# Kernel tuning notes

Measured on AMD Instinct MI355X. Metric: run time of the kernel, lower is better.

Reference implementation:

```python
import jax
jax.config.update("jax_enable_x64", True)  # hash math needs int64, as in the TF source
import jax.numpy as jnp
import numpy as np

NUM_LEVELS = 16
LEVEL_DIM = 2
BASE_RES = 16
HASHMAP_SIZE = 2 ** 19
N_POINTS = 1048576


def setup_inputs() -> dict:
    key = jax.random.key(0)
    k1, k2 = jax.random.split(key)
    # raw coords in [-size, size] with size=1.0 (forward normalizes to [0,1))
    x = jax.random.uniform(k1, (N_POINTS, 3), dtype=jnp.float32, minval=-1.0, maxval=1.0)
    # stacked per-level hash tables, init U(-1e-4, 1e-4) as in the keras layer
    tables = jax.random.uniform(
        k2, (NUM_LEVELS, HASHMAP_SIZE, LEVEL_DIM), dtype=jnp.float32,
        minval=-1e-4, maxval=1e-4)
    return {"x": x, "tables": tables}


def reference(x, tables):
    size = 1.0
    xn = jnp.clip((x + size) / (2.0 * size), 0.0, 1.0 - 1e-6)  # [N,3] in [0,1)
    primes = jnp.array([1546061, 1005013, 1673733], dtype=jnp.int64)  # per-axis hash primes
    offsets = jnp.array(
        [[0, 0, 0], [0, 0, 1], [0, 1, 0], [0, 1, 1],
         [1, 0, 0], [1, 0, 1], [1, 1, 0], [1, 1, 1]], dtype=jnp.int64)  # [8,3] cube corners
    is_one = offsets == 1  # [8,3]

    outs = []
    for lvl in range(NUM_LEVELS):  # fixed small unroll over resolution levels
        res = float(BASE_RES * (2 ** lvl))
        scaled = xn * res                      # [N,3]
        fl = jnp.floor(scaled)
        frac = scaled - fl                     # [N,3]
        corners = fl.astype(jnp.int64)[:, None, :] + offsets[None]      # [N,8,3]
        h = (jnp.sum(corners * primes, axis=-1) ^ lvl) % HASHMAP_SIZE   # [N,8]
        emb = tables[lvl][h]                   # gather -> [N,8,LEVEL_DIM]
        # trilinear weights: prod over axes of frac (if corner bit==1) else 1-frac
        w = jnp.prod(jnp.where(is_one[None], frac[:, None, :], 1.0 - frac[:, None, :]),
                     axis=-1)                  # [N,8]
        outs.append(jnp.sum(emb * w[..., None], axis=1))  # [N,LEVEL_DIM]
    return jnp.concatenate(outs, axis=-1)      # [N, NUM_LEVELS*LEVEL_DIM]
```

## Files before the change

### kernel.cpp

```cpp
#include <hip/hip_runtime.h>


#define NUM_LEVELS 16
#define HASHMAP_SIZE (1u << 19)
#define HASH_MASK (HASHMAP_SIZE - 1u)
#define BASE_RES 16
#define NXCD 8

template <bool DIRECT>
__global__ __launch_bounds__(256) void hash_level_kernel(
    const float* __restrict__ x,
    const float* __restrict__ tables,
    float* __restrict__ dst,
    int n, int nchunk) {
  const int b = blockIdx.x;
  const int lvl_lo = b % NXCD;
  const int r = b / NXCD;
  const int chunk = r % nchunk;
  const int lvl_hi = r / nchunk;
  const int lvl = lvl_lo + NXCD * lvl_hi;

  const int i = chunk * 256 + (int)threadIdx.x;
  if (i >= n) return;

  const unsigned P0 = 1546061u, P1 = 1005013u, P2 = 1673733u;
  const float UB = (float)(1.0 - 1e-6);

  const float px = x[3 * (size_t)i + 0];
  const float py = x[3 * (size_t)i + 1];
  const float pz = x[3 * (size_t)i + 2];

  const float xn0 = fminf(fmaxf((px + 1.0f) * 0.5f, 0.0f), UB);
  const float xn1 = fminf(fmaxf((py + 1.0f) * 0.5f, 0.0f), UB);
  const float xn2 = fminf(fmaxf((pz + 1.0f) * 0.5f, 0.0f), UB);

  const float res = (float)(BASE_RES << lvl);
  const float s0 = xn0 * res;
  const float s1 = xn1 * res;
  const float s2 = xn2 * res;
  const float f0 = floorf(s0);
  const float f1 = floorf(s1);
  const float f2 = floorf(s2);
  const float fr0 = s0 - f0, fr1 = s1 - f1, fr2 = s2 - f2;
  const unsigned c0 = (unsigned)f0, c1 = (unsigned)f1, c2 = (unsigned)f2;

  const unsigned base = c0 * P0 + c1 * P1 + c2 * P2;
  const float2* __restrict__ tbl =
      (const float2*)(tables + (size_t)lvl * HASHMAP_SIZE * 2);
  const float g0 = 1.0f - fr0, g1 = 1.0f - fr1, g2 = 1.0f - fr2;

  float acc0 = 0.0f, acc1 = 0.0f;
#pragma unroll
  for (int corner = 0; corner < 8; ++corner) {
    unsigned h = base;
    float w = 1.0f;
    if (corner & 4) { h += P0; w *= fr0; } else { w *= g0; }
    if (corner & 2) { h += P1; w *= fr1; } else { w *= g1; }
    if (corner & 1) { h += P2; w *= fr2; } else { w *= g2; }
    h = (h & HASH_MASK) ^ (unsigned)lvl;
    const float2 e = tbl[h];
    acc0 += e.x * w;
    acc1 += e.y * w;
  }

  if (DIRECT) {
    float2* o = (float2*)(dst + (size_t)i * (2 * NUM_LEVELS) + 2 * lvl);
    *o = make_float2(acc0, acc1);
  } else {
    float2 v = make_float2(acc0, acc1);
    double* p = (double*)(dst + ((size_t)lvl * n + i) * 2);
    __builtin_nontemporal_store(*(const double*)&v, p);
  }
}

__global__ __launch_bounds__(256) void transpose_kernel(
    const float* __restrict__ ws,
    float* __restrict__ out,
    int n) {
  const int i = blockIdx.x * blockDim.x + threadIdx.x;
  if (i >= n) return;

  float outv[2 * NUM_LEVELS];
#pragma unroll
  for (int lvl = 0; lvl < NUM_LEVELS; ++lvl) {
    const double* p = (const double*)(ws + ((size_t)lvl * n + i) * 2);
    double d = __builtin_nontemporal_load(p);
    ((double*)outv)[lvl] = d;
  }
  float4* o = (float4*)(out + (size_t)i * (2 * NUM_LEVELS));
#pragma unroll
  for (int k = 0; k < 8; ++k) o[k] = ((const float4*)outv)[k];
}

extern "C" void kernel_launch(void* const* d_in, const int* in_sizes, int n_in,
                              void* d_out, int out_size, void* d_ws, size_t ws_size,
                              hipStream_t stream) {
  const float* x = (const float*)d_in[0];
  const float* tables = (const float*)d_in[1];
  float* out = (float*)d_out;
  const int n = in_sizes[0] / 3;

  const int block = 256;
  const int nchunk = (n + block - 1) / block;
  const int nblocks = nchunk * NUM_LEVELS;

  const size_t ws_needed = (size_t)NUM_LEVELS * n * 2 * sizeof(float);
  if (ws_size >= ws_needed) {
    float* ws = (float*)d_ws;
    hash_level_kernel<false><<<nblocks, block, 0, stream>>>(x, tables, ws, n, nchunk);
    transpose_kernel<<<nchunk, block, 0, stream>>>(ws, out, n);
  } else {
    hash_level_kernel<true><<<nblocks, block, 0, stream>>>(x, tables, out, n, nchunk);
  }
}
```

Measured before the change: 655.2 us.

## Balance levels across XCDs with cost-weighted schedule and fp16 workspace

Replaces the fixed level-to-XCD block mapping with a host-built schedule that packs level/chunk segments onto each XCD using per-level cost estimates, so that cheaper coarse levels do not leave some XCDs idle. The intermediate workspace is stored as packed half2 instead of float2, halving the traffic of the staging write and the transpose read, and the x loads become nontemporal. Storing intermediates in fp16 loses precision in the output, and the schedule is built on the host on every launch.

New measurement: 772.3 us. 1.18x slower.

```diff
diff --git a/kernel.cpp b/kernel.cpp
--- a/kernel.cpp
+++ b/kernel.cpp
@@ -1,4 +1,5 @@
 #include <hip/hip_runtime.h>
+#include <hip/hip_fp16.h>
 
 
 #define NUM_LEVELS 16
@@ -6,19 +7,35 @@
 #define HASH_MASK (HASHMAP_SIZE - 1u)
 #define BASE_RES 16
 #define NXCD 8
-
-template <bool DIRECT>
+#define MAX_SEG 8
+
+struct Sched {
+  int j_end[NXCD][MAX_SEG];
+  int lvl[NXCD][MAX_SEG];
+  int c0[NXCD][MAX_SEG];
+  int nseg[NXCD];
+  int J;
+};
+
 __global__ __launch_bounds__(256) void hash_level_kernel(
     const float* __restrict__ x,
     const float* __restrict__ tables,
-    float* __restrict__ dst,
-    int n, int nchunk) {
-  const int b = blockIdx.x;
-  const int lvl_lo = b % NXCD;
-  const int r = b / NXCD;
-  const int chunk = r % nchunk;
-  const int lvl_hi = r / nchunk;
-  const int lvl = lvl_lo + NXCD * lvl_hi;
+    unsigned* __restrict__ ws,
+    int n, Sched s) {
+  const int xcd = blockIdx.x % NXCD;
+  const int j = blockIdx.x / NXCD;
+
+  int lvl = -1, chunk = 0, beg = 0;
+  const int ns = s.nseg[xcd];
+  for (int k = 0; k < ns; ++k) {
+    const int end = s.j_end[xcd][k];
+    if (j >= beg && j < end) {
+      lvl = s.lvl[xcd][k];
+      chunk = s.c0[xcd][k] + (j - beg);
+    }
+    beg = end;
+  }
+  if (lvl < 0) return;
 
   const int i = chunk * 256 + (int)threadIdx.x;
   if (i >= n) return;
@@ -26,21 +43,17 @@
   const unsigned P0 = 1546061u, P1 = 1005013u, P2 = 1673733u;
   const float UB = (float)(1.0 - 1e-6);
 
-  const float px = x[3 * (size_t)i + 0];
-  const float py = x[3 * (size_t)i + 1];
-  const float pz = x[3 * (size_t)i + 2];
+  const float px = __builtin_nontemporal_load(x + 3 * (size_t)i + 0);
+  const float py = __builtin_nontemporal_load(x + 3 * (size_t)i + 1);
+  const float pz = __builtin_nontemporal_load(x + 3 * (size_t)i + 2);
 
   const float xn0 = fminf(fmaxf((px + 1.0f) * 0.5f, 0.0f), UB);
   const float xn1 = fminf(fmaxf((py + 1.0f) * 0.5f, 0.0f), UB);
   const float xn2 = fminf(fmaxf((pz + 1.0f) * 0.5f, 0.0f), UB);
 
   const float res = (float)(BASE_RES << lvl);
-  const float s0 = xn0 * res;
-  const float s1 = xn1 * res;
-  const float s2 = xn2 * res;
-  const float f0 = floorf(s0);
-  const float f1 = floorf(s1);
-  const float f2 = floorf(s2);
+  const float s0 = xn0 * res, s1 = xn1 * res, s2 = xn2 * res;
+  const float f0 = floorf(s0), f1 = floorf(s1), f2 = floorf(s2);
   const float fr0 = s0 - f0, fr1 = s1 - f1, fr2 = s2 - f2;
   const unsigned c0 = (unsigned)f0, c1 = (unsigned)f1, c2 = (unsigned)f2;
 
@@ -63,18 +76,13 @@
     acc1 += e.y * w;
   }
 
-  if (DIRECT) {
-    float2* o = (float2*)(dst + (size_t)i * (2 * NUM_LEVELS) + 2 * lvl);
-    *o = make_float2(acc0, acc1);
-  } else {
-    float2 v = make_float2(acc0, acc1);
-    double* p = (double*)(dst + ((size_t)lvl * n + i) * 2);
-    __builtin_nontemporal_store(*(const double*)&v, p);
-  }
+  const __half2 h2 = __floats2half2_rn(acc0, acc1);
+  __builtin_nontemporal_store(*(const unsigned*)&h2,
+                              ws + (size_t)lvl * n + i);
 }
 
 __global__ __launch_bounds__(256) void transpose_kernel(
-    const float* __restrict__ ws,
+    const unsigned* __restrict__ ws,
     float* __restrict__ out,
     int n) {
   const int i = blockIdx.x * blockDim.x + threadIdx.x;
@@ -83,13 +91,103 @@
   float outv[2 * NUM_LEVELS];
 #pragma unroll
   for (int lvl = 0; lvl < NUM_LEVELS; ++lvl) {
-    const double* p = (const double*)(ws + ((size_t)lvl * n + i) * 2);
-    double d = __builtin_nontemporal_load(p);
-    ((double*)outv)[lvl] = d;
+    const unsigned u = __builtin_nontemporal_load(ws + (size_t)lvl * n + i);
+    const __half2 h2 = *(const __half2*)&u;
+    const float2 f = __half22float2(h2);
+    outv[2 * lvl + 0] = f.x;
+    outv[2 * lvl + 1] = f.y;
   }
   float4* o = (float4*)(out + (size_t)i * (2 * NUM_LEVELS));
 #pragma unroll
   for (int k = 0; k < 8; ++k) o[k] = ((const float4*)outv)[k];
+}
+
+__global__ __launch_bounds__(256) void hash_direct_kernel(
+    const float* __restrict__ x, const float* __restrict__ tables,
+    float* __restrict__ out, int n, int nchunk) {
+  const int b = blockIdx.x;
+  const int lvl_lo = b % NXCD;
+  const int r = b / NXCD;
+  const int chunk = r % nchunk;
+  const int lvl = lvl_lo + NXCD * (r / nchunk);
+  const int i = chunk * 256 + (int)threadIdx.x;
+  if (i >= n) return;
+
+  const unsigned P0 = 1546061u, P1 = 1005013u, P2 = 1673733u;
+  const float UB = (float)(1.0 - 1e-6);
+  const float px = x[3 * (size_t)i + 0];
+  const float py = x[3 * (size_t)i + 1];
+  const float pz = x[3 * (size_t)i + 2];
+  const float xn0 = fminf(fmaxf((px + 1.0f) * 0.5f, 0.0f), UB);
+  const float xn1 = fminf(fmaxf((py + 1.0f) * 0.5f, 0.0f), UB);
+  const float xn2 = fminf(fmaxf((pz + 1.0f) * 0.5f, 0.0f), UB);
+  const float res = (float)(BASE_RES << lvl);
+  const float s0 = xn0 * res, s1 = xn1 * res, s2 = xn2 * res;
+  const float f0 = floorf(s0), f1 = floorf(s1), f2 = floorf(s2);
+  const float fr0 = s0 - f0, fr1 = s1 - f1, fr2 = s2 - f2;
+  const unsigned base =
+      (unsigned)f0 * P0 + (unsigned)f1 * P1 + (unsigned)f2 * P2;
+  const float2* __restrict__ tbl =
+      (const float2*)(tables + (size_t)lvl * HASHMAP_SIZE * 2);
+  const float g0 = 1.0f - fr0, g1 = 1.0f - fr1, g2 = 1.0f - fr2;
+  float acc0 = 0.0f, acc1 = 0.0f;
+#pragma unroll
+  for (int corner = 0; corner < 8; ++corner) {
+    unsigned h = base;
+    float w = 1.0f;
+    if (corner & 4) { h += P0; w *= fr0; } else { w *= g0; }
+    if (corner & 2) { h += P1; w *= fr1; } else { w *= g1; }
+    if (corner & 1) { h += P2; w *= fr2; } else { w *= g2; }
+    h = (h & HASH_MASK) ^ (unsigned)lvl;
+    const float2 e = tbl[h];
+    acc0 += e.x * w;
+    acc1 += e.y * w;
+  }
+  float2* o = (float2*)(out + (size_t)i * (2 * NUM_LEVELS) + 2 * lvl);
+  *o = make_float2(acc0, acc1);
+}
+
+static void build_sched(Sched* s, int nchunk) {
+  const double c[NUM_LEVELS] = {0.5, 0.85, 0.95, 1, 1, 1, 1, 1,
+                                1,   1,    1,    1, 1, 1, 1, 1};
+  double total = 0;
+  for (int l = 0; l < NUM_LEVELS; ++l) total += c[l] * nchunk;
+  const double target = total / NXCD;
+
+  for (int xx = 0; xx < NXCD; ++xx) s->nseg[xx] = 0;
+  int xcd = 0;
+  double acc = 0;
+  for (int l = 0; l < NUM_LEVELS; ++l) {
+    int cpos = 0;
+    while (cpos < nchunk) {
+      int take;
+      if (xcd >= NXCD - 1) {
+        take = nchunk - cpos;
+      } else {
+        const double room = target - acc;
+        take = (int)(room / c[l] + 0.999999);
+        if (take > nchunk - cpos) take = nchunk - cpos;
+        if (take <= 0) { ++xcd; acc = 0; continue; }
+      }
+      int k = s->nseg[xcd];
+      if (k >= MAX_SEG) k = MAX_SEG - 1;
+      const int beg = (k == 0) ? 0 : s->j_end[xcd][k - 1];
+      s->j_end[xcd][k] = beg + take;
+      s->lvl[xcd][k] = l;
+      s->c0[xcd][k] = cpos;
+      s->nseg[xcd] = k + 1;
+      cpos += take;
+      acc += (double)take * c[l];
+      if (xcd < NXCD - 1 && acc >= target - 1e-6) { ++xcd; acc = 0; }
+    }
+  }
+  int J = 0;
+  for (int xx = 0; xx < NXCD; ++xx) {
+    const int k = s->nseg[xx];
+    const int e = k ? s->j_end[xx][k - 1] : 0;
+    if (e > J) J = e;
+  }
+  s->J = J;
 }
 
 extern "C" void kernel_launch(void* const* d_in, const int* in_sizes, int n_in,
@@ -102,14 +200,16 @@
 
   const int block = 256;
   const int nchunk = (n + block - 1) / block;
-  const int nblocks = nchunk * NUM_LEVELS;
-
-  const size_t ws_needed = (size_t)NUM_LEVELS * n * 2 * sizeof(float);
+
+  const size_t ws_needed = (size_t)NUM_LEVELS * n * sizeof(unsigned);
   if (ws_size >= ws_needed) {
-    float* ws = (float*)d_ws;
-    hash_level_kernel<false><<<nblocks, block, 0, stream>>>(x, tables, ws, n, nchunk);
+    Sched s;
+    build_sched(&s, nchunk);
+    unsigned* ws = (unsigned*)d_ws;
+    hash_level_kernel<<<NXCD * s.J, block, 0, stream>>>(x, tables, ws, n, s);
     transpose_kernel<<<nchunk, block, 0, stream>>>(ws, out, n);
   } else {
-    hash_level_kernel<true><<<nblocks, block, 0, stream>>>(x, tables, out, n, nchunk);
-  }
-}
+    hash_direct_kernel<<<nchunk * NUM_LEVELS, block, 0, stream>>>(
+        x, tables, out, n, nchunk);
+  }
+}
```
